# Kernel tuning notes

Hardware: AMD Instinct MI355X
Metric: run time of the kernel (lower is better)

Reference implementation:

```python
import jax, jax.numpy as jnp
import numpy as np

ALPHA = 0.2  # leaky_relu negative slope
NEG_INF = -1e9


def setup_inputs() -> dict:
    key = jax.random.key(0)
    ks = jax.random.split(key, 8)
    B, U, N, Din, H, HD = 8, 1024, 2048, 128, 4, 32
    return {
        "user_features": jax.random.normal(ks[0], (B, U, Din), jnp.float32),
        "news_features": jax.random.normal(ks[1], (B, N, Din), jnp.float32),
        "adjacency": jax.random.randint(ks[2], (B, U + N, U + N), 0, 2, jnp.int32),
        "W_user": jax.random.normal(ks[3], (H, Din, HD), jnp.float32) * 0.1,
        "W_news": jax.random.normal(ks[4], (H, Din, HD), jnp.float32) * 0.1,
        "a_user_news": jax.random.normal(ks[5], (H, 2 * HD, 1), jnp.float32) * 0.1,
        "a_news_user": jax.random.normal(ks[6], (H, 2 * HD, 1), jnp.float32) * 0.1,
        "b_user": jnp.zeros((H * HD,), jnp.float32),
        "b_news": jnp.zeros((H * HD,), jnp.float32),
    }


def _attention(q, k, a, mask):
    # q: (B,H,Q,hd), k: (B,H,K,hd), a: (H,2*hd,1), mask: (B,Q,K)
    # Additive score decomposed: [q;k] @ a == q@a_q + k@a_k (same math,
    # avoids materializing the (B,H,Q,K,2hd) concat tensor).
    hd = q.shape[-1]
    a_q = a[:, :hd, 0]  # (H,hd)
    a_k = a[:, hd:, 0]  # (H,hd)
    e_q = jnp.einsum("bhqd,hd->bhq", q, a_q)
    e_k = jnp.einsum("bhkd,hd->bhk", k, a_k)
    scores = e_q[..., :, None] + e_k[..., None, :]  # (B,H,Q,K)
    scores = jnp.where(scores > 0, scores, ALPHA * scores)  # leaky_relu
    scores = jnp.where(mask[:, None, :, :] > 0, scores, NEG_INF)
    return jax.nn.softmax(scores, axis=-1)


def reference(user_features, news_features, adjacency, W_user, W_news,
              a_user_news, a_news_user, b_user, b_news):
    B, U, _ = user_features.shape
    N = news_features.shape[1]
    units = b_user.shape[0]
    user_to_news = adjacency[:, :U, U:]   # (B,U,N)
    news_to_user = adjacency[:, U:, :U]   # (B,N,U)

    q_user = jnp.einsum("bud,hdk->bhuk", user_features, W_user)  # (B,H,U,hd)
    k_news = jnp.einsum("bnd,hdk->bhnk", news_features, W_news)  # (B,H,N,hd)

    attn_un = _attention(q_user, k_news, a_user_news, user_to_news)  # (B,H,U,N)
    user_updates = jnp.einsum("bhun,bhnk->bhuk", attn_un, k_news)

    attn_nu = _attention(k_news, q_user, a_news_user, news_to_user)  # (B,H,N,U)
    news_updates = jnp.einsum("bhnu,bhuk->bhnk", attn_nu, q_user)

    # concat_heads=True: original does a raw reshape of (B,H,*,hd) -> (B,*,units)
    updated_users = jnp.reshape(user_updates, (B, U, units)) + b_user
    updated_news = jnp.reshape(news_updates, (B, N, units)) + b_news
    updated_users = jax.nn.relu(updated_users)
    updated_news = jax.nn.relu(updated_news)
    return updated_users, updated_news
```

## Files before the change

### kernel.cpp

```cpp
#include <hip/hip_runtime.h>
#include <hip/hip_bf16.h>

typedef _Float16 half8 __attribute__((ext_vector_type(8)));
typedef __fp16 fp16x2 __attribute__((ext_vector_type(2)));
typedef float f32x4 __attribute__((ext_vector_type(4)));

#define B_ 8
#define U_ 1024
#define N_ 2048
#define DIN 128
#define H_ 4
#define HD 32
#define S_ 3072
#define LOG2E 1.44269504f

__global__ __launch_bounds__(256) void p0_kernel(
    const int* __restrict__ adj,
    unsigned int* __restrict__ mA, unsigned int* __restrict__ mB)
{
  const int task = blockIdx.x * 4 + (threadIdx.x >> 6);
  const int l = threadIdx.x & 63;
  const int* rowp;
  unsigned int* mOut;
  int iters;
  if (task < 8192) {
    int b = task >> 10, r = task & 1023;
    rowp = adj + ((size_t)b * S_ + r) * S_ + U_;
    iters = 32;
    mOut = mA + ((size_t)(b * 64 + (r >> 4)) * 64) * 16 + (r & 15);
  } else {
    int t2 = task - 8192;
    int b = t2 >> 11, r = t2 & 2047;
    rowp = adj + ((size_t)b * S_ + U_ + r) * S_;
    iters = 16;
    mOut = mB + ((size_t)(b * 128 + (r >> 4)) * 32) * 16 + (r & 15);
  }
  #pragma unroll 4
  for (int it = 0; it < iters; ++it) {
    int av = rowp[it * 64 + l];
    unsigned long long m = __ballot(av != 0);
    if (l == 0) {
      mOut[(2 * it) * 16]     = (unsigned int)m;
      mOut[(2 * it + 1) * 16] = (unsigned int)(m >> 32);
    }
  }
}

__global__ __launch_bounds__(256) void p1_kernel(
    const float* __restrict__ uf, const float* __restrict__ nf,
    const float* __restrict__ Wu, const float* __restrict__ Wn,
    const float* __restrict__ a_un, const float* __restrict__ a_nu,
    _Float16* __restrict__ vtA, _Float16* __restrict__ vtB,
    float* __restrict__ eRowA, float2* __restrict__ eColA2,
    float* __restrict__ eRowB, float2* __restrict__ eColB2)
{
  __shared__ float fs[64][132];
  __shared__ float WsT[32][132];
  __shared__ float qt[32][65];
  __shared__ float aAs[32], aBs[32];

  const int bid = blockIdx.x;
  const int tid = threadIdx.x;

  int b, rt, R, h;
  const float *feat, *W;
  _Float16* vt;
  float* eRaw;
  float2* ePair;
  bool part0raw;
  int aAoff, aBoff;
  const float *avA, *avB;
  if (bid < 512) {
    h = bid & 3; int t2 = bid >> 2; b = t2 >> 4; rt = t2 & 15; R = U_;
    feat = uf; W = Wu; vt = vtB;
    eRaw = eRowA; ePair = eColB2; part0raw = true;
    avA = a_un; aAoff = 0;  avB = a_nu; aBoff = HD;
  } else {
    int t3 = bid - 512;
    h = t3 & 3; int t2 = t3 >> 2; b = t2 >> 5; rt = t2 & 31; R = N_;
    feat = nf; W = Wn; vt = vtA;
    eRaw = eRowB; ePair = eColA2; part0raw = false;
    avA = a_un; aAoff = HD; avB = a_nu; aBoff = 0;
  }
  const int r0 = rt * 64;

  const float4* feat4 = (const float4*)(feat + ((size_t)b * R + r0) * DIN);
  #pragma unroll
  for (int i = 0; i < 8; ++i) {
    int f4 = tid + 256 * i;
    int row = f4 >> 5, c4 = f4 & 31;
    *(float4*)&fs[row][c4 * 4] = feat4[row * 32 + c4];
  }
  {
    const float4* W4 = (const float4*)(W + (size_t)h * DIN * HD);
    #pragma unroll
    for (int i = 0; i < 4; ++i) {
      int f4 = tid + 256 * i;
      int d = f4 >> 3, kc = f4 & 7;
      float4 v = W4[f4];
      WsT[kc * 4 + 0][d] = v.x;
      WsT[kc * 4 + 1][d] = v.y;
      WsT[kc * 4 + 2][d] = v.z;
      WsT[kc * 4 + 3][d] = v.w;
    }
    if (tid < 32) {
      aAs[tid] = avA[h * 64 + aAoff + tid];
      aBs[tid] = avB[h * 64 + aBoff + tid];
    }
  }
  __syncthreads();

  const int kk = tid & 15, uu = tid >> 4;
  {
    float acc0[4] = {0.f, 0.f, 0.f, 0.f}, acc1[4] = {0.f, 0.f, 0.f, 0.f};
    #pragma unroll 8
    for (int d = 0; d < DIN; d += 4) {
      float4 w0 = *(const float4*)&WsT[kk][d];
      float4 w1 = *(const float4*)&WsT[kk + 16][d];
      #pragma unroll
      for (int i = 0; i < 4; ++i) {
        float4 fv = *(const float4*)&fs[uu + 16 * i][d];
        acc0[i] = fmaf(fv.x, w0.x, acc0[i]); acc0[i] = fmaf(fv.y, w0.y, acc0[i]);
        acc0[i] = fmaf(fv.z, w0.z, acc0[i]); acc0[i] = fmaf(fv.w, w0.w, acc0[i]);
        acc1[i] = fmaf(fv.x, w1.x, acc1[i]); acc1[i] = fmaf(fv.y, w1.y, acc1[i]);
        acc1[i] = fmaf(fv.z, w1.z, acc1[i]); acc1[i] = fmaf(fv.w, w1.w, acc1[i]);
      }
    }
    #pragma unroll
    for (int i = 0; i < 4; ++i) {
      qt[kk][uu + 16 * i] = acc0[i];
      qt[kk + 16][uu + 16 * i] = acc1[i];
    }
  }
  __syncthreads();

  const int u2 = tid & 63, part = tid >> 6;
  {
    size_t vtbase = (size_t)(b * H_ + h) * (R * HD)
                  + (size_t)((r0 >> 5) + (u2 >> 5)) * (HD * 32) + (u2 & 31);
    #pragma unroll
    for (int jj = 0; jj < 8; ++jj) {
      int krow = part * 8 + jj;
      vt[vtbase + krow * 32] = (_Float16)qt[krow][u2];
    }
  }
  if (part < 2) {
    float a_ = 0.f;
    const float* av = (part == 0) ? aAs : aBs;
    #pragma unroll
    for (int k2 = 0; k2 < HD; ++k2)
      a_ = fmaf(qt[k2][u2], av[k2], a_);
    float e = a_ * LOG2E;
    size_t idx = (size_t)(b * H_ + h) * R + r0 + u2;
    bool raw = (part == 0) ? part0raw : !part0raw;
    if (raw) eRaw[idx] = e;
    else     ePair[idx] = make_float2(exp2f(e), exp2f(0.2f * e));
  }
}

struct Tile { float4 e0, e1, e2, e3; half8 v0, v1; unsigned int m32; };

__device__ __forceinline__ Tile load_tile(
    int t, int cg, int row16,
    const float2* __restrict__ ecol2, const _Float16* __restrict__ vtb,
    const unsigned int* __restrict__ mT)
{
  Tile ti;
  const int cb = t * 32 + cg;
  const float4* ep = (const float4*)(ecol2 + cb);
  ti.e0 = ep[0]; ti.e1 = ep[1]; ti.e2 = ep[2]; ti.e3 = ep[3];
  ti.v0 = *(const half8*)(vtb + t * (HD * 32) + row16 * 32 + cg);
  ti.v1 = *(const half8*)(vtb + t * (HD * 32) + (row16 + 16) * 32 + cg);
  ti.m32 = mT[t * 16 + row16];
  return ti;
}

__device__ __forceinline__ void compute_tile(
    const Tile& ti, int cg, float F1, float F2, float G, half8 ones,
    f32x4& acc0, f32x4& acc1, f32x4& accd)
{
  const unsigned int mb = ti.m32 >> cg;
  float wv[8];
  wv[0] = (mb & 1u)   ? (ti.e0.x > G ? ti.e0.x * F1 : ti.e0.y * F2) : 0.f;
  wv[1] = (mb & 2u)   ? (ti.e0.z > G ? ti.e0.z * F1 : ti.e0.w * F2) : 0.f;
  wv[2] = (mb & 4u)   ? (ti.e1.x > G ? ti.e1.x * F1 : ti.e1.y * F2) : 0.f;
  wv[3] = (mb & 8u)   ? (ti.e1.z > G ? ti.e1.z * F1 : ti.e1.w * F2) : 0.f;
  wv[4] = (mb & 16u)  ? (ti.e2.x > G ? ti.e2.x * F1 : ti.e2.y * F2) : 0.f;
  wv[5] = (mb & 32u)  ? (ti.e2.z > G ? ti.e2.z * F1 : ti.e2.w * F2) : 0.f;
  wv[6] = (mb & 64u)  ? (ti.e3.x > G ? ti.e3.x * F1 : ti.e3.y * F2) : 0.f;
  wv[7] = (mb & 128u) ? (ti.e3.z > G ? ti.e3.z * F1 : ti.e3.w * F2) : 0.f;
  union { fp16x2 h2[4]; half8 h8; } uw;
  uw.h2[0] = __builtin_amdgcn_cvt_pkrtz(wv[0], wv[1]);
  uw.h2[1] = __builtin_amdgcn_cvt_pkrtz(wv[2], wv[3]);
  uw.h2[2] = __builtin_amdgcn_cvt_pkrtz(wv[4], wv[5]);
  uw.h2[3] = __builtin_amdgcn_cvt_pkrtz(wv[6], wv[7]);
  half8 w = uw.h8;
  acc0 = __builtin_amdgcn_mfma_f32_16x16x32_f16(w, ti.v0, acc0, 0, 0, 0);
  acc1 = __builtin_amdgcn_mfma_f32_16x16x32_f16(w, ti.v1, acc1, 0, 0, 0);
  accd = __builtin_amdgcn_mfma_f32_16x16x32_f16(w, ones, accd, 0, 0, 0);
}

template<int RR, int CC>
__device__ __forceinline__ void p2_core(
    int b, int rt, int wave, int l,
    const unsigned int* __restrict__ mT, const _Float16* __restrict__ vt,
    const float* __restrict__ eRow, const float2* __restrict__ eCol2,
    const float* __restrict__ bias, float* __restrict__ out)
{
  const int h = wave;
  const int row16 = l & 15;
  const int cg = (l >> 4) << 3;
  const int r = rt * 16 + row16;
  const float eq = eRow[(size_t)(b * H_ + h) * RR + r];
  const float F1 = exp2f(eq), F2 = exp2f(0.2f * eq), G = exp2f(-eq);
  const float2* ecol2 = eCol2 + (size_t)(b * H_ + h) * CC;
  const _Float16* vtb = vt + (size_t)(b * H_ + h) * (CC * HD);

  f32x4 acc0 = {0.f,0.f,0.f,0.f}, acc1 = {0.f,0.f,0.f,0.f}, accd = {0.f,0.f,0.f,0.f};
  half8 ones = {(_Float16)1.f, (_Float16)1.f, (_Float16)1.f, (_Float16)1.f,
                (_Float16)1.f, (_Float16)1.f, (_Float16)1.f, (_Float16)1.f};

  constexpr int T = CC / 32;
  Tile cur = load_tile(0, cg, row16, ecol2, vtb, mT);
  #pragma unroll 2
  for (int t = 0; t < T - 1; ++t) {
    Tile nxt = load_tile(t + 1, cg, row16, ecol2, vtb, mT);
    compute_tile(cur, cg, F1, F2, G, ones, acc0, acc1, accd);
    cur = nxt;
  }
  compute_tile(cur, cg, F1, F2, G, ones, acc0, acc1, accd);

  const int colk = row16;
  const int rowbase = rt * 16 + ((l >> 4) << 2);
  #pragma unroll
  for (int q = 0; q < 4; ++q) {
    int orow = rowbase + q;
    size_t o = ((size_t)(b * H_ + h) * RR + orow) * 32 + colk;
    float den = accd[q];
    float v0 = acc0[q] / den + bias[q * 32 + colk];
    float v1 = acc1[q] / den + bias[q * 32 + colk + 16];
    out[o]      = v0 > 0.f ? v0 : 0.f;
    out[o + 16] = v1 > 0.f ? v1 : 0.f;
  }
}

__global__ __launch_bounds__(256, 4) void p2_kernel(
    const unsigned int* __restrict__ mA, const unsigned int* __restrict__ mB,
    const _Float16* __restrict__ vtA, const _Float16* __restrict__ vtB,
    const float* __restrict__ eRowA, const float2* __restrict__ eColA2,
    const float* __restrict__ eRowB, const float2* __restrict__ eColB2,
    const float* __restrict__ bu, const float* __restrict__ bn,
    float* __restrict__ out)
{
  const int tid = threadIdx.x;
  const int wave = tid >> 6, l = tid & 63;
  const int bid = blockIdx.x;
  if (bid < B_ * (U_ / 16)) {
    const int b = bid & 7, rt = bid >> 3;
    const unsigned int* mT = mA + ((size_t)(b * 64 + rt) * 64) * 16;
    p2_core<U_, N_>(b, rt, wave, l, mT, vtA, eRowA, eColA2, bu, out);
  } else {
    const int t2 = bid - B_ * (U_ / 16);
    const int b = t2 & 7, rt = t2 >> 3;
    const unsigned int* mT = mB + ((size_t)(b * 128 + rt) * 32) * 16;
    p2_core<N_, U_>(b, rt, wave, l, mT, vtB, eRowB, eColB2, bn,
                    out + (size_t)B_ * U_ * 128);
  }
}

extern "C" void kernel_launch(void* const* d_in, const int* in_sizes, int n_in,
                              void* d_out, int out_size, void* d_ws, size_t ws_size,
                              hipStream_t stream) {
  const float* uf  = (const float*)d_in[0];
  const float* nf  = (const float*)d_in[1];
  const int*   adj = (const int*)d_in[2];
  const float* Wu  = (const float*)d_in[3];
  const float* Wn  = (const float*)d_in[4];
  const float* aun = (const float*)d_in[5];
  const float* anu = (const float*)d_in[6];
  const float* bu  = (const float*)d_in[7];
  const float* bn  = (const float*)d_in[8];

  char* ws = (char*)d_ws;
  size_t off = 0;
  _Float16* vtA = (_Float16*)(ws + off); off += (size_t)B_ * H_ * HD * N_ * 2;
  _Float16* vtB = (_Float16*)(ws + off); off += (size_t)B_ * H_ * HD * U_ * 2;
  float*  eRowA  = (float*)(ws + off);  off += (size_t)B_ * H_ * U_ * 4;
  float2* eColA2 = (float2*)(ws + off); off += (size_t)B_ * H_ * N_ * 8;
  float*  eRowB  = (float*)(ws + off);  off += (size_t)B_ * H_ * N_ * 4;
  float2* eColB2 = (float2*)(ws + off); off += (size_t)B_ * H_ * U_ * 8;
  unsigned int* mA = (unsigned int*)(ws + off); off += (size_t)B_ * 64 * 64 * 16 * 4;
  unsigned int* mB = (unsigned int*)(ws + off); off += (size_t)B_ * 128 * 32 * 16 * 4;
  (void)off; (void)ws_size; (void)in_sizes; (void)n_in; (void)out_size;

  p0_kernel<<<6144, 256, 0, stream>>>(adj, mA, mB);
  p1_kernel<<<512 + 1024, 256, 0, stream>>>(uf, nf, Wu, Wn, aun, anu,
                                            vtA, vtB, eRowA, eColA2, eRowB, eColB2);
  p2_kernel<<<B_ * (U_ / 16) + B_ * (N_ / 16), 256, 0, stream>>>(
      mA, mB, vtA, vtB, eRowA, eColA2, eRowB, eColB2, bu, bn, (float*)d_out);
}
```

Baseline: 136.1 us.

## Split user-side attention across key halves and compute exp in-loop

The user-to-news pass is split into two blocks per row tile, each covering half of the news columns. Partial numerators and denominators go to workspace, and a new p3 kernel combines them with bias and ReLU. This balances per-block work with the news-to-user pass, which already loops over 32 tiles. The precomputed exp pairs are replaced by direct exp2 of the leaky-relu score inside the loop, which halves the column-score bytes read but adds eight exp2 per tile. The explicit load prefetch and the occupancy hint in the launch bounds are dropped. The extra kernel launch and the partial-sum round trip through global memory add overhead.

```diff
diff --git a/kernel.cpp b/kernel.cpp
--- a/kernel.cpp
+++ b/kernel.cpp
@@ -13,6 +13,7 @@
 #define HD 32
 #define S_ 3072
 #define LOG2E 1.44269504f
+#define NU (B_ * U_ * 128)
 
 __global__ __launch_bounds__(256) void p0_kernel(
     const int* __restrict__ adj,
@@ -51,8 +52,8 @@
     const float* __restrict__ Wu, const float* __restrict__ Wn,
     const float* __restrict__ a_un, const float* __restrict__ a_nu,
     _Float16* __restrict__ vtA, _Float16* __restrict__ vtB,
-    float* __restrict__ eRowA, float2* __restrict__ eColA2,
-    float* __restrict__ eRowB, float2* __restrict__ eColB2)
+    float* __restrict__ eRowA, float* __restrict__ eColA,
+    float* __restrict__ eRowB, float* __restrict__ eColB)
 {
   __shared__ float fs[64][132];
   __shared__ float WsT[32][132];
@@ -65,21 +66,19 @@
   int b, rt, R, h;
   const float *feat, *W;
   _Float16* vt;
-  float* eRaw;
-  float2* ePair;
-  bool part0raw;
+  float *eA, *eB;
   int aAoff, aBoff;
   const float *avA, *avB;
   if (bid < 512) {
     h = bid & 3; int t2 = bid >> 2; b = t2 >> 4; rt = t2 & 15; R = U_;
     feat = uf; W = Wu; vt = vtB;
-    eRaw = eRowA; ePair = eColB2; part0raw = true;
+    eA = eRowA; eB = eColB;
     avA = a_un; aAoff = 0;  avB = a_nu; aBoff = HD;
   } else {
     int t3 = bid - 512;
     h = t3 & 3; int t2 = t3 >> 2; b = t2 >> 5; rt = t2 & 31; R = N_;
     feat = nf; W = Wn; vt = vtA;
-    eRaw = eRowB; ePair = eColA2; part0raw = false;
+    eA = eColA; eB = eRowB;
     avA = a_un; aAoff = HD; avB = a_nu; aBoff = 0;
   }
   const int r0 = rt * 64;
@@ -150,122 +149,121 @@
     #pragma unroll
     for (int k2 = 0; k2 < HD; ++k2)
       a_ = fmaf(qt[k2][u2], av[k2], a_);
-    float e = a_ * LOG2E;
-    size_t idx = (size_t)(b * H_ + h) * R + r0 + u2;
-    bool raw = (part == 0) ? part0raw : !part0raw;
-    if (raw) eRaw[idx] = e;
-    else     ePair[idx] = make_float2(exp2f(e), exp2f(0.2f * e));
-  }
-}
-
-struct Tile { float4 e0, e1, e2, e3; half8 v0, v1; unsigned int m32; };
-
-__device__ __forceinline__ Tile load_tile(
-    int t, int cg, int row16,
-    const float2* __restrict__ ecol2, const _Float16* __restrict__ vtb,
-    const unsigned int* __restrict__ mT)
+    float* e = (part == 0) ? eA : eB;
+    e[(size_t)(b * H_ + h) * R + r0 + u2] = a_ * LOG2E;
+  }
+}
+
+__global__ __launch_bounds__(256) void p2_kernel(
+    const unsigned int* __restrict__ mA, const unsigned int* __restrict__ mB,
+    const _Float16* __restrict__ vtA, const _Float16* __restrict__ vtB,
+    const float* __restrict__ eRowA, const float* __restrict__ eColA,
+    const float* __restrict__ eRowB, const float* __restrict__ eColB,
+    const float* __restrict__ bu, const float* __restrict__ bn,
+    float* __restrict__ numA, float* __restrict__ denA,
+    float* __restrict__ out)
 {
-  Tile ti;
-  const int cb = t * 32 + cg;
-  const float4* ep = (const float4*)(ecol2 + cb);
-  ti.e0 = ep[0]; ti.e1 = ep[1]; ti.e2 = ep[2]; ti.e3 = ep[3];
-  ti.v0 = *(const half8*)(vtb + t * (HD * 32) + row16 * 32 + cg);
-  ti.v1 = *(const half8*)(vtb + t * (HD * 32) + (row16 + 16) * 32 + cg);
-  ti.m32 = mT[t * 16 + row16];
-  return ti;
-}
-
-__device__ __forceinline__ void compute_tile(
-    const Tile& ti, int cg, float F1, float F2, float G, half8 ones,
-    f32x4& acc0, f32x4& acc1, f32x4& accd)
-{
-  const unsigned int mb = ti.m32 >> cg;
-  float wv[8];
-  wv[0] = (mb & 1u)   ? (ti.e0.x > G ? ti.e0.x * F1 : ti.e0.y * F2) : 0.f;
-  wv[1] = (mb & 2u)   ? (ti.e0.z > G ? ti.e0.z * F1 : ti.e0.w * F2) : 0.f;
-  wv[2] = (mb & 4u)   ? (ti.e1.x > G ? ti.e1.x * F1 : ti.e1.y * F2) : 0.f;
-  wv[3] = (mb & 8u)   ? (ti.e1.z > G ? ti.e1.z * F1 : ti.e1.w * F2) : 0.f;
-  wv[4] = (mb & 16u)  ? (ti.e2.x > G ? ti.e2.x * F1 : ti.e2.y * F2) : 0.f;
-  wv[5] = (mb & 32u)  ? (ti.e2.z > G ? ti.e2.z * F1 : ti.e2.w * F2) : 0.f;
-  wv[6] = (mb & 64u)  ? (ti.e3.x > G ? ti.e3.x * F1 : ti.e3.y * F2) : 0.f;
-  wv[7] = (mb & 128u) ? (ti.e3.z > G ? ti.e3.z * F1 : ti.e3.w * F2) : 0.f;
-  union { fp16x2 h2[4]; half8 h8; } uw;
-  uw.h2[0] = __builtin_amdgcn_cvt_pkrtz(wv[0], wv[1]);
-  uw.h2[1] = __builtin_amdgcn_cvt_pkrtz(wv[2], wv[3]);
-  uw.h2[2] = __builtin_amdgcn_cvt_pkrtz(wv[4], wv[5]);
-  uw.h2[3] = __builtin_amdgcn_cvt_pkrtz(wv[6], wv[7]);
-  half8 w = uw.h8;
-  acc0 = __builtin_amdgcn_mfma_f32_16x16x32_f16(w, ti.v0, acc0, 0, 0, 0);
-  acc1 = __builtin_amdgcn_mfma_f32_16x16x32_f16(w, ti.v1, acc1, 0, 0, 0);
-  accd = __builtin_amdgcn_mfma_f32_16x16x32_f16(w, ones, accd, 0, 0, 0);
-}
-
-template<int RR, int CC>
-__device__ __forceinline__ void p2_core(
-    int b, int rt, int wave, int l,
-    const unsigned int* __restrict__ mT, const _Float16* __restrict__ vt,
-    const float* __restrict__ eRow, const float2* __restrict__ eCol2,
-    const float* __restrict__ bias, float* __restrict__ out)
-{
-  const int h = wave;
+  const int tid = threadIdx.x;
+  const int h = tid >> 6, l = tid & 63;
   const int row16 = l & 15;
   const int cg = (l >> 4) << 3;
-  const int r = rt * 16 + row16;
-  const float eq = eRow[(size_t)(b * H_ + h) * RR + r];
-  const float F1 = exp2f(eq), F2 = exp2f(0.2f * eq), G = exp2f(-eq);
-  const float2* ecol2 = eCol2 + (size_t)(b * H_ + h) * CC;
-  const _Float16* vtb = vt + (size_t)(b * H_ + h) * (CC * HD);
+  const int bid = blockIdx.x;
 
   f32x4 acc0 = {0.f,0.f,0.f,0.f}, acc1 = {0.f,0.f,0.f,0.f}, accd = {0.f,0.f,0.f,0.f};
   half8 ones = {(_Float16)1.f, (_Float16)1.f, (_Float16)1.f, (_Float16)1.f,
                 (_Float16)1.f, (_Float16)1.f, (_Float16)1.f, (_Float16)1.f};
 
-  constexpr int T = CC / 32;
-  Tile cur = load_tile(0, cg, row16, ecol2, vtb, mT);
+  const float* ecolH;
+  const _Float16* vtb;
+  const unsigned int* mT;
+  float eq;
+  int t0;
+  if (bid < 1024) {
+    const int b = bid & 7, rest = bid >> 3;
+    const int rt = rest & 63, g = rest >> 6;
+    eq = eRowA[(size_t)(b * H_ + h) * U_ + rt * 16 + row16];
+    ecolH = eColA + (size_t)(b * H_ + h) * N_;
+    vtb = vtA + (size_t)(b * H_ + h) * (N_ * HD);
+    mT = mA + ((size_t)(b * 64 + rt) * 64) * 16;
+    t0 = g * 32;
+  } else {
+    const int t2 = bid - 1024;
+    const int b = t2 & 7, rt = t2 >> 3;
+    eq = eRowB[(size_t)(b * H_ + h) * N_ + rt * 16 + row16];
+    ecolH = eColB + (size_t)(b * H_ + h) * U_;
+    vtb = vtB + (size_t)(b * H_ + h) * (U_ * HD);
+    mT = mB + ((size_t)(b * 128 + rt) * 32) * 16;
+    t0 = 0;
+  }
+
   #pragma unroll 2
-  for (int t = 0; t < T - 1; ++t) {
-    Tile nxt = load_tile(t + 1, cg, row16, ecol2, vtb, mT);
-    compute_tile(cur, cg, F1, F2, G, ones, acc0, acc1, accd);
-    cur = nxt;
-  }
-  compute_tile(cur, cg, F1, F2, G, ones, acc0, acc1, accd);
+  for (int tt = 0; tt < 32; ++tt) {
+    const int t = t0 + tt;
+    const int cb = t * 32 + cg;
+    unsigned int mb = mT[t * 16 + row16] >> cg;
+    float4 e0 = *(const float4*)(ecolH + cb);
+    float4 e1 = *(const float4*)(ecolH + cb + 4);
+    float ecv[8] = {e0.x, e0.y, e0.z, e0.w, e1.x, e1.y, e1.z, e1.w};
+    float wv[8];
+    #pragma unroll
+    for (int j = 0; j < 8; ++j) {
+      float s  = eq + ecv[j];
+      float ls = fmaxf(s, 0.2f * s);
+      ls = (mb & (1u << j)) ? ls : -1e9f;
+      wv[j] = exp2f(ls);
+    }
+    union { fp16x2 h2[4]; half8 h8; } uw;
+    uw.h2[0] = __builtin_amdgcn_cvt_pkrtz(wv[0], wv[1]);
+    uw.h2[1] = __builtin_amdgcn_cvt_pkrtz(wv[2], wv[3]);
+    uw.h2[2] = __builtin_amdgcn_cvt_pkrtz(wv[4], wv[5]);
+    uw.h2[3] = __builtin_amdgcn_cvt_pkrtz(wv[6], wv[7]);
+    half8 w = uw.h8;
+    const half8 v0 = *(const half8*)(vtb + t * (HD * 32) + row16 * 32 + cg);
+    const half8 v1 = *(const half8*)(vtb + t * (HD * 32) + (row16 + 16) * 32 + cg);
+    acc0 = __builtin_amdgcn_mfma_f32_16x16x32_f16(w, v0, acc0, 0, 0, 0);
+    acc1 = __builtin_amdgcn_mfma_f32_16x16x32_f16(w, v1, acc1, 0, 0, 0);
+    accd = __builtin_amdgcn_mfma_f32_16x16x32_f16(w, ones, accd, 0, 0, 0);
+  }
 
   const int colk = row16;
-  const int rowbase = rt * 16 + ((l >> 4) << 2);
-  #pragma unroll
-  for (int q = 0; q < 4; ++q) {
-    int orow = rowbase + q;
-    size_t o = ((size_t)(b * H_ + h) * RR + orow) * 32 + colk;
-    float den = accd[q];
-    float v0 = acc0[q] / den + bias[q * 32 + colk];
-    float v1 = acc1[q] / den + bias[q * 32 + colk + 16];
-    out[o]      = v0 > 0.f ? v0 : 0.f;
-    out[o + 16] = v1 > 0.f ? v1 : 0.f;
-  }
-}
-
-__global__ __launch_bounds__(256, 4) void p2_kernel(
-    const unsigned int* __restrict__ mA, const unsigned int* __restrict__ mB,
-    const _Float16* __restrict__ vtA, const _Float16* __restrict__ vtB,
-    const float* __restrict__ eRowA, const float2* __restrict__ eColA2,
-    const float* __restrict__ eRowB, const float2* __restrict__ eColB2,
-    const float* __restrict__ bu, const float* __restrict__ bn,
-    float* __restrict__ out)
+  const int g4 = (l >> 4) << 2;
+  if (bid < 1024) {
+    const int b = bid & 7, rest = bid >> 3;
+    const int rt = rest & 63, g = rest >> 6;
+    #pragma unroll
+    for (int q = 0; q < 4; ++q) {
+      int orow = rt * 16 + g4 + q;
+      size_t o = (((size_t)(g * 8 + b) * H_ + h) * U_ + orow) * 32 + colk;
+      numA[o] = acc0[q];
+      numA[o + 16] = acc1[q];
+      if (colk == 0) denA[((size_t)(g * 8 + b) * H_ + h) * U_ + orow] = accd[q];
+    }
+  } else {
+    const int t2 = bid - 1024;
+    const int b = t2 & 7, rt = t2 >> 3;
+    #pragma unroll
+    for (int q = 0; q < 4; ++q) {
+      int orow = rt * 16 + g4 + q;
+      size_t o = ((size_t)(b * H_ + h) * N_ + orow) * 32 + colk;
+      float den = accd[q];
+      float v0 = acc0[q] / den + bn[q * 32 + colk];
+      float v1 = acc1[q] / den + bn[q * 32 + colk + 16];
+      out[NU + o]      = v0 > 0.f ? v0 : 0.f;
+      out[NU + o + 16] = v1 > 0.f ? v1 : 0.f;
+    }
+  }
+}
+
+__global__ __launch_bounds__(256) void p3_kernel(
+    const float* __restrict__ numA, const float* __restrict__ denA,
+    const float* __restrict__ bu, float* __restrict__ out)
 {
-  const int tid = threadIdx.x;
-  const int wave = tid >> 6, l = tid & 63;
-  const int bid = blockIdx.x;
-  if (bid < B_ * (U_ / 16)) {
-    const int b = bid & 7, rt = bid >> 3;
-    const unsigned int* mT = mA + ((size_t)(b * 64 + rt) * 64) * 16;
-    p2_core<U_, N_>(b, rt, wave, l, mT, vtA, eRowA, eColA2, bu, out);
-  } else {
-    const int t2 = bid - B_ * (U_ / 16);
-    const int b = t2 & 7, rt = t2 >> 3;
-    const unsigned int* mT = mB + ((size_t)(b * 128 + rt) * 32) * 16;
-    p2_core<N_, U_>(b, rt, wave, l, mT, vtB, eRowB, eColB2, bn,
-                    out + (size_t)B_ * U_ * 128);
-  }
+  int idx = blockIdx.x * 256 + threadIdx.x;
+  float n = numA[idx] + numA[idx + NU];
+  int dr = idx >> 5;
+  float d = denA[dr] + denA[dr + B_ * H_ * U_];
+  float v = n / d + bu[idx & 127];
+  out[idx] = v > 0.f ? v : 0.f;
 }
 
 extern "C" void kernel_launch(void* const* d_in, const int* in_sizes, int n_in,
@@ -285,17 +283,20 @@
   size_t off = 0;
   _Float16* vtA = (_Float16*)(ws + off); off += (size_t)B_ * H_ * HD * N_ * 2;
   _Float16* vtB = (_Float16*)(ws + off); off += (size_t)B_ * H_ * HD * U_ * 2;
-  float*  eRowA  = (float*)(ws + off);  off += (size_t)B_ * H_ * U_ * 4;
-  float2* eColA2 = (float2*)(ws + off); off += (size_t)B_ * H_ * N_ * 8;
-  float*  eRowB  = (float*)(ws + off);  off += (size_t)B_ * H_ * N_ * 4;
-  float2* eColB2 = (float2*)(ws + off); off += (size_t)B_ * H_ * U_ * 8;
+  float* eRowA = (float*)(ws + off); off += (size_t)B_ * H_ * U_ * 4;
+  float* eColA = (float*)(ws + off); off += (size_t)B_ * H_ * N_ * 4;
+  float* eRowB = (float*)(ws + off); off += (size_t)B_ * H_ * N_ * 4;
+  float* eColB = (float*)(ws + off); off += (size_t)B_ * H_ * U_ * 4;
   unsigned int* mA = (unsigned int*)(ws + off); off += (size_t)B_ * 64 * 64 * 16 * 4;
   unsigned int* mB = (unsigned int*)(ws + off); off += (size_t)B_ * 128 * 32 * 16 * 4;
+  float* numA = (float*)(ws + off); off += (size_t)2 * NU * 4;
+  float* denA = (float*)(ws + off); off += (size_t)2 * B_ * H_ * U_ * 4;
   (void)off; (void)ws_size; (void)in_sizes; (void)n_in; (void)out_size;
 
   p0_kernel<<<6144, 256, 0, stream>>>(adj, mA, mB);
   p1_kernel<<<512 + 1024, 256, 0, stream>>>(uf, nf, Wu, Wn, aun, anu,
-                                            vtA, vtB, eRowA, eColA2, eRowB, eColB2);
-  p2_kernel<<<B_ * (U_ / 16) + B_ * (N_ / 16), 256, 0, stream>>>(
-      mA, mB, vtA, vtB, eRowA, eColA2, eRowB, eColB2, bu, bn, (float*)d_out);
-}
+                                            vtA, vtB, eRowA, eColA, eRowB, eColB);
+  p2_kernel<<<2048, 256, 0, stream>>>(mA, mB, vtA, vtB, eRowA, eColA,
+                                      eRowB, eColB, bu, bn, numA, denA, (float*)d_out);
+  p3_kernel<<<NU / 256, 256, 0, stream>>>(numA, denA, bu, (float*)d_out);
+}
```

New measurement: 122.3 us. -10.2%, faster.
